# Optimization experiments

Hardware: AMD Instinct MI355X
Metric: run time of the kernel (lower is better)

The kernel has to match this reference:

```python
import jax, jax.numpy as jnp
import numpy as np

H = 2048
N = 2_097_152
BINS = 256


def _tensor2image(x):
    # de-normalize from [-1,1]-style to [0,1] (SCGAN's tensor2image)
    return x * 0.5 + 0.5


def _cdf(vals):
    # torch.histc(vals, bins=256, min=0, max=256): unit-width bins; values here lie in [0,256)
    b = jnp.clip(jnp.floor(vals), 0, BINS - 1).astype(jnp.int32)
    hist = jnp.zeros((BINS,), jnp.float32).at[b].add(1.0)
    c = jnp.cumsum(hist)
    return c / c[BINS - 1]


def _trans_table(ref_cdf, adj_cdf):
    # table[i] = first j in 1..255 with adj[j-1] <= ref[i] <= adj[j]; else i. table[0]=0, table[255]=255.
    r = ref_cdf[:, None]                # [256,1]
    lo = adj_cdf[None, :-1]             # adj[j-1], j=1..255
    hi = adj_cdf[None, 1:]              # adj[j]
    cond = (lo <= r) & (r <= hi)        # [256,255]
    found = jnp.any(cond, axis=1)
    j_first = 1 + jnp.argmax(cond, axis=1)
    table = jnp.where(found, j_first, jnp.arange(BINS))
    table = table.at[0].set(0).at[BINS - 1].set(BINS - 1)
    return table


def _histogram_matching(dst_img, ref_img, i0, i1, i2, i3):
    dst_align = dst_img[:, i0, i1]      # [3,N]
    ref_align = ref_img[:, i2, i3]      # [3,N]
    cdf_dst = jax.vmap(_cdf)(dst_align)           # [3,256]
    cdf_ref = jax.vmap(_cdf)(ref_align)           # [3,256]
    tables = jax.vmap(_trans_table)(cdf_dst, cdf_ref)  # [3,256] int
    ix = jnp.clip(jnp.floor(dst_align), 0, BINS - 1).astype(jnp.int32)
    matched = jnp.take_along_axis(tables, ix, axis=1).astype(dst_img.dtype)  # [3,N]
    return dst_img.at[:, i0, i1].set(matched)


def setup_inputs() -> dict:
    key = jax.random.key(0)
    ks = jax.random.split(key, 9)
    return {
        "input_data": jax.random.uniform(ks[0], (1, 3, H, H), jnp.float32),
        "target_data": jax.random.uniform(ks[1], (1, 3, H, H), jnp.float32),
        "mask_src": jax.random.randint(ks[2], (1, 1, H, H), 0, 2).astype(jnp.float32),
        "mask_tar": jax.random.randint(ks[3], (1, 1, H, H), 0, 2).astype(jnp.float32),
        "idx0": jax.random.randint(ks[4], (N,), 0, H),
        "idx1": jax.random.randint(ks[5], (N,), 0, H),
        "idx2": jax.random.randint(ks[6], (N,), 0, H),
        "idx3": jax.random.randint(ks[7], (N,), 0, H),
        "ref": jax.random.uniform(ks[8], (1, 3, H, H), jnp.float32),
    }


def reference(input_data, target_data, mask_src, mask_tar, idx0, idx1, idx2, idx3, ref):
    img = _tensor2image(input_data)[0] * 255.0   # [3,H,H]
    tgt = _tensor2image(target_data)[0] * 255.0  # [3,H,H]
    rf = _tensor2image(ref)[0] * 255.0           # [3,H,H]
    m_src = jnp.broadcast_to(mask_src[0, 0], img.shape)
    m_tar = jnp.broadcast_to(mask_tar[0, 0], tgt.shape)
    input_masked = img * m_src
    target_masked = tgt * m_tar
    ref_masked = rf * m_src
    match = jax.lax.stop_gradient(
        _histogram_matching(ref_masked, target_masked, idx0, idx1, idx2, idx3)
    ) * m_src
    return jnp.mean(jnp.abs(input_masked - match))
```

## Files before the change

### kernel.cpp

```cpp
#include <hip/hip_runtime.h>

#define H 2048
#define HH (H * H)
#define NIDX 2097152
#define BINS 256
#define CH 3

#define NBUCK 64
#define NLIST 128
#define CAPG  139264
#define WS_HIST_DST 0
#define WS_HIST_REF 3072
#define WS_TABLE    6144
#define WS_ACC      9216
#define WS_CURS     9728
#define WS_CTRL_BYTES 16384
#define WS_SEL      16384
#define WS_BPS      (16384 + (size_t)HH)
#define WS_BPR      (WS_BPS + (size_t)HH * 4)
#define WS_LIST     (WS_BPR + (size_t)HH * 4)
#define WS_MAIN_BYTES (WS_LIST + (size_t)NLIST * CAPG * 2)

#define FB_CNT_DST  16384
#define FB_BINPACK  (16384 + (size_t)HH * 2)
#define FB_ZERO_BYTES (16384 + (size_t)HH * 2)

__device__ __forceinline__ int bin_of(float v) {
    int b = (int)floorf(v);
    return min(max(b, 0), BINS - 1);
}


__global__ __launch_bounds__(256) void prep_main(
    const float* __restrict__ mask_src, const float* __restrict__ mask_tar,
    const float* __restrict__ refimg, const float* __restrict__ tgtimg,
    unsigned int* __restrict__ bps, unsigned int* __restrict__ bpr,
    unsigned int* __restrict__ sel4)
{
    const int nq = HH / 4;
    const int stride = gridDim.x * 256;
    for (int q = blockIdx.x * 256 + threadIdx.x; q < nq; q += stride) {
        float4 ms4 = ((const float4*)mask_src)[q];
        float4 mt4 = ((const float4*)mask_tar)[q];
        const float ms[4] = { ms4.x, ms4.y, ms4.z, ms4.w };
        const float mt[4] = { mt4.x, mt4.y, mt4.z, mt4.w };
        unsigned int wsrc[4] = { 0u, 0u, 0u, 0u };
        unsigned int wref[4] = { 0u, 0u, 0u, 0u };
        #pragma unroll
        for (int c = 0; c < CH; ++c) {
            float4 r4 = ((const float4*)(refimg + (size_t)c * HH))[q];
            float4 t4 = ((const float4*)(tgtimg + (size_t)c * HH))[q];
            const float rr[4] = { r4.x, r4.y, r4.z, r4.w };
            const float tt[4] = { t4.x, t4.y, t4.z, t4.w };
            #pragma unroll
            for (int e = 0; e < 4; ++e) {
                float vs = (rr[e] * 0.5f + 0.5f) * 255.0f * ms[e];
                float vt = (tt[e] * 0.5f + 0.5f) * 255.0f * mt[e];
                wsrc[e] |= ((unsigned int)bin_of(vs)) << (8 * c);
                wref[e] |= ((unsigned int)bin_of(vt)) << (8 * c);
            }
        }
        uint4 o1 = { wsrc[0], wsrc[1], wsrc[2], wsrc[3] };
        uint4 o2 = { wref[0], wref[1], wref[2], wref[3] };
        ((uint4*)bps)[q] = o1;
        ((uint4*)bpr)[q] = o2;
        sel4[q] = 0u;
    }
}

#define P1_BLOCKS 512
#define P1_SPB (NIDX / P1_BLOCKS)
#define P1_CAP 128

__global__ __launch_bounds__(256) void partition_kernel(
    const int* __restrict__ idx0, const int* __restrict__ idx1,
    const int* __restrict__ idx2, const int* __restrict__ idx3,
    unsigned short* __restrict__ list_g, unsigned int* __restrict__ curs)
{
    __shared__ unsigned short stage[NLIST * P1_CAP];
    __shared__ unsigned int lcnt[NLIST];
    __shared__ unsigned int lbase[NLIST];
    for (int i = threadIdx.x; i < NLIST; i += 256) lcnt[i] = 0u;
    __syncthreads();

    const int base_k = blockIdx.x * P1_SPB;
    for (int r = 0; r < P1_SPB / 256; ++r) {
        int k = base_k + r * 256 + threadIdx.x;
        int pd = idx0[k] * H + idx1[k];
        int pr = idx2[k] * H + idx3[k];
        {
            int l = pd >> 16;
            unsigned int pos = atomicAdd(&lcnt[l], 1u);
            if (pos < P1_CAP) stage[l * P1_CAP + pos] = (unsigned short)(pd & 0xFFFF);
            else {
                unsigned int g = atomicAdd(&curs[l], 1u);
                if (g < CAPG) list_g[(size_t)l * CAPG + g] = (unsigned short)(pd & 0xFFFF);
            }
        }
        {
            int l = 64 + (pr >> 16);
            unsigned int pos = atomicAdd(&lcnt[l], 1u);
            if (pos < P1_CAP) stage[l * P1_CAP + pos] = (unsigned short)(pr & 0xFFFF);
            else {
                unsigned int g = atomicAdd(&curs[l], 1u);
                if (g < CAPG) list_g[(size_t)l * CAPG + g] = (unsigned short)(pr & 0xFFFF);
            }
        }
    }
    __syncthreads();
    if (threadIdx.x < NLIST) {
        unsigned int n = min(lcnt[threadIdx.x], (unsigned int)P1_CAP);
        lbase[threadIdx.x] = atomicAdd(&curs[threadIdx.x], n);
    }
    __syncthreads();
    for (int b = 0; b < NLIST; ++b) {
        int n = (int)min(lcnt[b], (unsigned int)P1_CAP);
        unsigned int gb = lbase[b];
        for (int e = threadIdx.x; e < n; e += 256) {
            unsigned int gi = gb + e;
            if (gi < CAPG) list_g[(size_t)b * CAPG + gi] = stage[b * P1_CAP + e];
        }
    }
}

__global__ __launch_bounds__(256) void gather_hist_kernel(
    const unsigned short* __restrict__ list_g, const unsigned int* __restrict__ curs,
    const unsigned int* __restrict__ bps, const unsigned int* __restrict__ bpr,
    unsigned char* __restrict__ selected,
    unsigned int* __restrict__ hist_dst, unsigned int* __restrict__ hist_ref)
{
    __shared__ unsigned int hd[CH * BINS];
    __shared__ unsigned int hr[CH * BINS];
    for (int i = threadIdx.x; i < CH * BINS; i += 256) { hd[i] = 0u; hr[i] = 0u; }
    __syncthreads();

    const int xcd = blockIdx.x & 7;
    const int j = blockIdx.x >> 3;
    unsigned int zc_d = 0, zc_r = 0;

    for (int phase = 0; phase < 8; ++phase) {
        const int bucket = xcd * 8 + phase;
        const unsigned int pbase = ((unsigned int)bucket) << 16;
        {
            const int l = bucket;
            unsigned int n = min(curs[l], (unsigned int)CAPG);
            unsigned int chunk = (n + 255u) >> 8;
            unsigned int s = j * chunk;
            unsigned int e = min(s + chunk, n);
            for (unsigned int i = s + threadIdx.x; i < e; i += 256) {
                unsigned int p = pbase | (unsigned int)list_g[(size_t)l * CAPG + i];
                unsigned int w = bps[p];
                selected[p] = 1;
                if (w == 0u) ++zc_d;
                else {
                    atomicAdd(&hd[0 * BINS + (w & 0xFFu)], 1u);
                    atomicAdd(&hd[1 * BINS + ((w >> 8) & 0xFFu)], 1u);
                    atomicAdd(&hd[2 * BINS + ((w >> 16) & 0xFFu)], 1u);
                }
            }
        }
        {
            const int l = 64 + bucket;
            unsigned int n = min(curs[l], (unsigned int)CAPG);
            unsigned int chunk = (n + 255u) >> 8;
            unsigned int s = j * chunk;
            unsigned int e = min(s + chunk, n);
            for (unsigned int i = s + threadIdx.x; i < e; i += 256) {
                unsigned int p = pbase | (unsigned int)list_g[(size_t)l * CAPG + i];
                unsigned int w = bpr[p];
                if (w == 0u) ++zc_r;
                else {
                    atomicAdd(&hr[0 * BINS + (w & 0xFFu)], 1u);
                    atomicAdd(&hr[1 * BINS + ((w >> 8) & 0xFFu)], 1u);
                    atomicAdd(&hr[2 * BINS + ((w >> 16) & 0xFFu)], 1u);
                }
            }
        }
    }

    int zd = (int)zc_d, zr = (int)zc_r;
    #pragma unroll
    for (int off = 32; off; off >>= 1) { zd += __shfl_down(zd, off); zr += __shfl_down(zr, off); }
    if ((threadIdx.x & 63) == 0) {
        if (zd) {
            atomicAdd(&hd[0 * BINS], (unsigned int)zd);
            atomicAdd(&hd[1 * BINS], (unsigned int)zd);
            atomicAdd(&hd[2 * BINS], (unsigned int)zd);
        }
        if (zr) {
            atomicAdd(&hr[0 * BINS], (unsigned int)zr);
            atomicAdd(&hr[1 * BINS], (unsigned int)zr);
            atomicAdd(&hr[2 * BINS], (unsigned int)zr);
        }
    }

    __syncthreads();
    for (int i = threadIdx.x; i < CH * BINS; i += 256) {
        unsigned int v = hd[i];
        if (v) atomicAdd(&hist_dst[i], v);
        v = hr[i];
        if (v) atomicAdd(&hist_ref[i], v);
    }
}

__global__ __launch_bounds__(256) void table_kernel(
    const unsigned int* __restrict__ hist_dst,
    const unsigned int* __restrict__ hist_ref,
    int* __restrict__ table)
{
    __shared__ float cd[CH * BINS];
    __shared__ float cr[CH * BINS];
    __shared__ float wpart[4];
    const int i = threadIdx.x;
    const int lane = i & 63;
    const int wave = i >> 6;

    for (int a = 0; a < 6; ++a) {
        const unsigned int* h = (a < 3) ? (hist_dst + a * BINS) : (hist_ref + (a - 3) * BINS);
        float* out = (a < 3) ? (cd + a * BINS) : (cr + (a - 3) * BINS);
        float x = (float)h[i];
        #pragma unroll
        for (int off = 1; off < 64; off <<= 1) {
            float y = __shfl_up(x, off);
            if (lane >= off) x += y;
        }
        if (lane == 63) wpart[wave] = x;
        __syncthreads();
        float prefix = 0.0f;
        #pragma unroll
        for (int w = 0; w < 3; ++w) if (w < wave) prefix += wpart[w];
        x += prefix;
        float tot = wpart[0] + wpart[1] + wpart[2] + wpart[3];
        out[i] = x / tot;
        __syncthreads();
    }

    #pragma unroll
    for (int c = 0; c < CH; ++c) {
        int t;
        if (i == 0) t = 0;
        else if (i == BINS - 1) t = BINS - 1;
        else {
            float r = cd[c * BINS + i];
            int lo = 1, hi = BINS - 1;
            while (lo < hi) {
                int mid = (lo + hi) >> 1;
                if (cr[c * BINS + mid] < r) lo = mid + 1; else hi = mid;
            }
            t = (cr[c * BINS + lo - 1] <= r) ? lo : i;
        }
        table[c * BINS + i] = t;
    }
}

__global__ __launch_bounds__(256) void loss_sel_kernel(
    const float* __restrict__ input, const float* __restrict__ refimg,
    const float* __restrict__ mask_src, const unsigned char* __restrict__ selected,
    const int* __restrict__ table, double* __restrict__ acc)
{
    __shared__ int tab[CH * BINS];
    for (int i = threadIdx.x; i < CH * BINS; i += 256) tab[i] = table[i];
    __syncthreads();

    float lsum = 0.0f;
    const int nq = HH / 4;
    const int stride = gridDim.x * 256;
    for (int q = blockIdx.x * 256 + threadIdx.x; q < nq; q += stride) {
        float4 m4 = ((const float4*)mask_src)[q];
        uchar4 s4 = ((const uchar4*)selected)[q];
        const unsigned char ss[4] = { s4.x, s4.y, s4.z, s4.w };
        const float mm[4] = { m4.x, m4.y, m4.z, m4.w };
        #pragma unroll
        for (int c = 0; c < CH; ++c) {
            float4 a4 = ((const float4*)(input + (size_t)c * HH))[q];
            float4 r4 = ((const float4*)(refimg + (size_t)c * HH))[q];
            const float aa[4] = { a4.x, a4.y, a4.z, a4.w };
            const float rr[4] = { r4.x, r4.y, r4.z, r4.w };
            #pragma unroll
            for (int e = 0; e < 4; ++e) {
                float m = mm[e];
                float av = (aa[e] * 0.5f + 0.5f) * 255.0f * m;
                float rv = (rr[e] * 0.5f + 0.5f) * 255.0f * m;
                float tv = (float)tab[c * BINS + bin_of(rv)];
                float mv = m * (ss[e] ? tv : rv);
                lsum += fabsf(av - mv);
            }
        }
    }

    double d = (double)lsum;
    #pragma unroll
    for (int off = 32; off; off >>= 1) d += __shfl_down(d, off);
    __shared__ double wsum[4];
    int wid = threadIdx.x >> 6;
    int lane = threadIdx.x & 63;
    if (lane == 0) wsum[wid] = d;
    __syncthreads();
    if (threadIdx.x == 0) {
        double t = wsum[0] + wsum[1] + wsum[2] + wsum[3];
        atomicAdd(acc, t);
    }
}

__global__ void finalize_kernel(const double* __restrict__ acc, float* __restrict__ out)
{
    if (threadIdx.x == 0 && blockIdx.x == 0) {
        out[0] = (float)(acc[0] / (double)(CH * (double)HH));
    }
}


__device__ __forceinline__ void cnt_inc(unsigned int* cnt, int p) {
    atomicAdd(&cnt[p >> 1], (p & 1) ? 0x10000u : 1u);
}

__global__ __launch_bounds__(256) void fb_prep_kernel(
    const float* __restrict__ mask_tar, const float* __restrict__ tgtimg,
    unsigned int* __restrict__ binpack)
{
    const int nq = HH / 4;
    const int stride = gridDim.x * 256;
    for (int q = blockIdx.x * 256 + threadIdx.x; q < nq; q += stride) {
        float4 m4 = ((const float4*)mask_tar)[q];
        const float mm[4] = { m4.x, m4.y, m4.z, m4.w };
        unsigned int w[4] = { 0u, 0u, 0u, 0u };
        #pragma unroll
        for (int c = 0; c < CH; ++c) {
            float4 t4 = ((const float4*)(tgtimg + (size_t)c * HH))[q];
            const float tt[4] = { t4.x, t4.y, t4.z, t4.w };
            #pragma unroll
            for (int e = 0; e < 4; ++e) {
                float v = (tt[e] * 0.5f + 0.5f) * 255.0f * mm[e];
                w[e] |= ((unsigned int)bin_of(v)) << (8 * c);
            }
        }
        uint4 out = { w[0], w[1], w[2], w[3] };
        ((uint4*)binpack)[q] = out;
    }
}

__global__ __launch_bounds__(256) void fb_scatter_kernel(
    const int4* __restrict__ idx0, const int4* __restrict__ idx1,
    const int4* __restrict__ idx2, const int4* __restrict__ idx3,
    const unsigned int* __restrict__ binpack,
    unsigned int* __restrict__ cnt_dst, unsigned int* __restrict__ hist_ref)
{
    __shared__ unsigned int hr[CH * BINS];
    for (int i = threadIdx.x; i < CH * BINS; i += 256) hr[i] = 0u;
    __syncthreads();

    unsigned int zc = 0;
    const int n4 = NIDX / 4;
    const int stride = gridDim.x * 256;
    for (int k = blockIdx.x * 256 + threadIdx.x; k < n4; k += stride) {
        int4 a = idx0[k], b = idx1[k], c = idx2[k], d = idx3[k];
        int p0 = c.x * H + d.x, p1 = c.y * H + d.y;
        int p2 = c.z * H + d.z, p3 = c.w * H + d.w;
        unsigned int w0 = binpack[p0], w1 = binpack[p1];
        unsigned int w2 = binpack[p2], w3 = binpack[p3];

        cnt_inc(cnt_dst, a.x * H + b.x);
        cnt_inc(cnt_dst, a.y * H + b.y);
        cnt_inc(cnt_dst, a.z * H + b.z);
        cnt_inc(cnt_dst, a.w * H + b.w);

        const unsigned int ws2[4] = { w0, w1, w2, w3 };
        #pragma unroll
        for (int e = 0; e < 4; ++e) {
            unsigned int w = ws2[e];
            if (w == 0u) ++zc;
            else {
                atomicAdd(&hr[0 * BINS + (w & 0xFFu)], 1u);
                atomicAdd(&hr[1 * BINS + ((w >> 8) & 0xFFu)], 1u);
                atomicAdd(&hr[2 * BINS + ((w >> 16) & 0xFFu)], 1u);
            }
        }
    }

    int z = (int)zc;
    #pragma unroll
    for (int off = 32; off; off >>= 1) z += __shfl_down(z, off);
    if ((threadIdx.x & 63) == 0 && z) {
        atomicAdd(&hr[0 * BINS], (unsigned int)z);
        atomicAdd(&hr[1 * BINS], (unsigned int)z);
        atomicAdd(&hr[2 * BINS], (unsigned int)z);
    }

    __syncthreads();
    for (int i = threadIdx.x; i < CH * BINS; i += 256) {
        unsigned int v = hr[i];
        if (v) atomicAdd(&hist_ref[i], v);
    }
}

__global__ __launch_bounds__(256) void fb_sweep_kernel(
    const float* __restrict__ mask_src, const float* __restrict__ refimg,
    const unsigned int* __restrict__ cnt_dst,
    unsigned int* __restrict__ hist_dst)
{
    __shared__ unsigned int hd[CH * BINS];
    for (int i = threadIdx.x; i < CH * BINS; i += 256) hd[i] = 0u;
    __syncthreads();

    unsigned int zc = 0;
    const int nq = HH / 4;
    const int stride = gridDim.x * 256;
    for (int q = blockIdx.x * 256 + threadIdx.x; q < nq; q += stride) {
        uint2 wd = ((const uint2*)cnt_dst)[q];
        unsigned int cdc[4] = { wd.x & 0xFFFFu, wd.x >> 16, wd.y & 0xFFFFu, wd.y >> 16 };
        float4 ms4 = ((const float4*)mask_src)[q];
        const float ms[4] = { ms4.x, ms4.y, ms4.z, ms4.w };

        float rv[CH][4];
        #pragma unroll
        for (int c = 0; c < CH; ++c) {
            float4 r4 = ((const float4*)(refimg + (size_t)c * HH))[q];
            rv[c][0] = r4.x; rv[c][1] = r4.y; rv[c][2] = r4.z; rv[c][3] = r4.w;
        }
        #pragma unroll
        for (int e = 0; e < 4; ++e) {
            if (cdc[e]) {
                if (ms[e] == 0.0f) zc += cdc[e];
                else {
                    #pragma unroll
                    for (int c = 0; c < CH; ++c) {
                        float v = (rv[c][e] * 0.5f + 0.5f) * 255.0f;
                        atomicAdd(&hd[c * BINS + bin_of(v)], cdc[e]);
                    }
                }
            }
        }
    }

    int z = (int)zc;
    #pragma unroll
    for (int off = 32; off; off >>= 1) z += __shfl_down(z, off);
    if ((threadIdx.x & 63) == 0 && z) {
        atomicAdd(&hd[0 * BINS], (unsigned int)z);
        atomicAdd(&hd[1 * BINS], (unsigned int)z);
        atomicAdd(&hd[2 * BINS], (unsigned int)z);
    }

    __syncthreads();
    for (int i = threadIdx.x; i < CH * BINS; i += 256) {
        unsigned int v = hd[i];
        if (v) atomicAdd(&hist_dst[i], v);
    }
}

__global__ __launch_bounds__(256) void fb_loss_kernel(
    const float* __restrict__ input, const float* __restrict__ refimg,
    const float* __restrict__ mask_src, const unsigned int* __restrict__ cnt_dst,
    const int* __restrict__ table, double* __restrict__ acc)
{
    __shared__ int tab[CH * BINS];
    for (int i = threadIdx.x; i < CH * BINS; i += 256) tab[i] = table[i];
    __syncthreads();

    float lsum = 0.0f;
    const int nq = HH / 4;
    const int stride = gridDim.x * 256;
    for (int q = blockIdx.x * 256 + threadIdx.x; q < nq; q += stride) {
        float4 m4 = ((const float4*)mask_src)[q];
        uint2 w = ((const uint2*)cnt_dst)[q];
        const unsigned int sel[4] = { w.x & 0xFFFFu, w.x >> 16, w.y & 0xFFFFu, w.y >> 16 };
        const float mm[4] = { m4.x, m4.y, m4.z, m4.w };
        #pragma unroll
        for (int c = 0; c < CH; ++c) {
            float4 a4 = ((const float4*)(input + (size_t)c * HH))[q];
            float4 r4 = ((const float4*)(refimg + (size_t)c * HH))[q];
            const float aa[4] = { a4.x, a4.y, a4.z, a4.w };
            const float rr[4] = { r4.x, r4.y, r4.z, r4.w };
            #pragma unroll
            for (int e = 0; e < 4; ++e) {
                float m = mm[e];
                float av = (aa[e] * 0.5f + 0.5f) * 255.0f * m;
                float rv = (rr[e] * 0.5f + 0.5f) * 255.0f * m;
                float tv = (float)tab[c * BINS + bin_of(rv)];
                float mv = m * (sel[e] ? tv : rv);
                lsum += fabsf(av - mv);
            }
        }
    }

    double d = (double)lsum;
    #pragma unroll
    for (int off = 32; off; off >>= 1) d += __shfl_down(d, off);
    __shared__ double wsum[4];
    int wid = threadIdx.x >> 6;
    int lane = threadIdx.x & 63;
    if (lane == 0) wsum[wid] = d;
    __syncthreads();
    if (threadIdx.x == 0) {
        double t = wsum[0] + wsum[1] + wsum[2] + wsum[3];
        atomicAdd(acc, t);
    }
}


extern "C" void kernel_launch(void* const* d_in, const int* in_sizes, int n_in,
                              void* d_out, int out_size, void* d_ws, size_t ws_size,
                              hipStream_t stream)
{
    const float* input    = (const float*)d_in[0];
    const float* target   = (const float*)d_in[1];
    const float* mask_src = (const float*)d_in[2];
    const float* mask_tar = (const float*)d_in[3];
    const int*   idx0     = (const int*)d_in[4];
    const int*   idx1     = (const int*)d_in[5];
    const int*   idx2     = (const int*)d_in[6];
    const int*   idx3     = (const int*)d_in[7];
    const float* refimg   = (const float*)d_in[8];

    char* ws = (char*)d_ws;
    unsigned int* hist_dst = (unsigned int*)(ws + WS_HIST_DST);
    unsigned int* hist_ref = (unsigned int*)(ws + WS_HIST_REF);
    int*          table    = (int*)(ws + WS_TABLE);
    double*       acc      = (double*)(ws + WS_ACC);

    if (ws_size >= WS_MAIN_BYTES) {
        unsigned int*   curs     = (unsigned int*)(ws + WS_CURS);
        unsigned char*  selected = (unsigned char*)(ws + WS_SEL);
        unsigned int*   bps      = (unsigned int*)(ws + WS_BPS);
        unsigned int*   bpr      = (unsigned int*)(ws + WS_BPR);
        unsigned short* list_g   = (unsigned short*)(ws + WS_LIST);

        hipMemsetAsync(d_ws, 0, WS_CTRL_BYTES, stream);
        prep_main<<<2048, 256, 0, stream>>>(mask_src, mask_tar, refimg, target,
                                            bps, bpr, (unsigned int*)selected);
        partition_kernel<<<P1_BLOCKS, 256, 0, stream>>>(idx0, idx1, idx2, idx3,
                                                        list_g, curs);
        gather_hist_kernel<<<2048, 256, 0, stream>>>(list_g, curs, bps, bpr,
                                                     selected, hist_dst, hist_ref);
        table_kernel<<<1, 256, 0, stream>>>(hist_dst, hist_ref, table);
        loss_sel_kernel<<<2048, 256, 0, stream>>>(input, refimg, mask_src,
                                                  selected, table, acc);
        finalize_kernel<<<1, 64, 0, stream>>>(acc, (float*)d_out);
    } else {
        unsigned int* cnt_dst = (unsigned int*)(ws + FB_CNT_DST);
        unsigned int* binpack = (unsigned int*)(ws + FB_BINPACK);

        hipMemsetAsync(d_ws, 0, FB_ZERO_BYTES, stream);
        fb_prep_kernel<<<2048, 256, 0, stream>>>(mask_tar, target, binpack);
        fb_scatter_kernel<<<2048, 256, 0, stream>>>((const int4*)idx0, (const int4*)idx1,
                                                    (const int4*)idx2, (const int4*)idx3,
                                                    binpack, cnt_dst, hist_ref);
        fb_sweep_kernel<<<1024, 256, 0, stream>>>(mask_src, refimg, cnt_dst, hist_dst);
        table_kernel<<<1, 256, 0, stream>>>(hist_dst, hist_ref, table);
        fb_loss_kernel<<<2048, 256, 0, stream>>>(input, refimg, mask_src, cnt_dst,
                                                 table, acc);
        finalize_kernel<<<1, 64, 0, stream>>>(acc, (float*)d_out);
    }
}
```

Baseline: 351.1 us.

## Split gather-histogram work per block by side and bucket with vectorized list loads

New measurement: 328.5 us. -6.4%, faster.

```diff
diff --git a/kernel.cpp b/kernel.cpp
--- a/kernel.cpp
+++ b/kernel.cpp
@@ -129,77 +129,81 @@
     unsigned char* __restrict__ selected,
     unsigned int* __restrict__ hist_dst, unsigned int* __restrict__ hist_ref)
 {
-    __shared__ unsigned int hd[CH * BINS];
-    __shared__ unsigned int hr[CH * BINS];
-    for (int i = threadIdx.x; i < CH * BINS; i += 256) { hd[i] = 0u; hr[i] = 0u; }
-    __syncthreads();
-
-    const int xcd = blockIdx.x & 7;
-    const int j = blockIdx.x >> 3;
-    unsigned int zc_d = 0, zc_r = 0;
-
-    for (int phase = 0; phase < 8; ++phase) {
-        const int bucket = xcd * 8 + phase;
-        const unsigned int pbase = ((unsigned int)bucket) << 16;
-        {
-            const int l = bucket;
-            unsigned int n = min(curs[l], (unsigned int)CAPG);
-            unsigned int chunk = (n + 255u) >> 8;
-            unsigned int s = j * chunk;
-            unsigned int e = min(s + chunk, n);
-            for (unsigned int i = s + threadIdx.x; i < e; i += 256) {
-                unsigned int p = pbase | (unsigned int)list_g[(size_t)l * CAPG + i];
-                unsigned int w = bps[p];
-                selected[p] = 1;
-                if (w == 0u) ++zc_d;
+    __shared__ unsigned int hh[CH * BINS];
+    for (int i = threadIdx.x; i < CH * BINS; i += 256) hh[i] = 0u;
+    __syncthreads();
+
+    const int xcd  = blockIdx.x & 7;
+    const int j    = blockIdx.x >> 3;
+    const int bsl  = j & 15;
+    const int sub  = j >> 4;
+    const int side = bsl >> 3;
+    const int bucket = xcd * 8 + (bsl & 7);
+    const int l = side * 64 + bucket;
+    const unsigned int pbase = ((unsigned int)bucket) << 16;
+    const unsigned int* __restrict__ src = side ? bpr : bps;
+
+    const unsigned int n = min(curs[l], (unsigned int)CAPG);
+    const unsigned int chunk = (((n + 15u) >> 4) + 7u) & ~7u;
+    const unsigned int s = (unsigned int)sub * chunk;
+    const unsigned int e = min(s + chunk, n);
+    const unsigned short* lbase = list_g + (size_t)l * CAPG;
+
+    unsigned int zc = 0;
+    for (unsigned int ib = s + (unsigned int)threadIdx.x * 8u; ib < e; ib += 2048u) {
+        unsigned int w[8];
+        unsigned int pcnt;
+        if (ib + 8u <= e) {
+            uint4 raw = *(const uint4*)(lbase + ib);
+            const unsigned int ent[8] = {
+                raw.x & 0xFFFFu, raw.x >> 16, raw.y & 0xFFFFu, raw.y >> 16,
+                raw.z & 0xFFFFu, raw.z >> 16, raw.w & 0xFFFFu, raw.w >> 16 };
+            #pragma unroll
+            for (int k = 0; k < 8; ++k) {
+                unsigned int p = pbase | ent[k];
+                w[k] = src[p];
+                if (side == 0) selected[p] = 1;
+            }
+            pcnt = 8u;
+        } else {
+            pcnt = e - ib;
+            #pragma unroll
+            for (int k = 0; k < 8; ++k) {
+                if ((unsigned int)k < pcnt) {
+                    unsigned int p = pbase | (unsigned int)lbase[ib + k];
+                    w[k] = src[p];
+                    if (side == 0) selected[p] = 1;
+                } else w[k] = 0xFFFFFFFFu;
+            }
+        }
+        #pragma unroll
+        for (int k = 0; k < 8; ++k) {
+            if ((unsigned int)k < pcnt) {
+                unsigned int ww = w[k];
+                if (ww == 0u) ++zc;
                 else {
-                    atomicAdd(&hd[0 * BINS + (w & 0xFFu)], 1u);
-                    atomicAdd(&hd[1 * BINS + ((w >> 8) & 0xFFu)], 1u);
-                    atomicAdd(&hd[2 * BINS + ((w >> 16) & 0xFFu)], 1u);
+                    atomicAdd(&hh[0 * BINS + (ww & 0xFFu)], 1u);
+                    atomicAdd(&hh[1 * BINS + ((ww >> 8) & 0xFFu)], 1u);
+                    atomicAdd(&hh[2 * BINS + ((ww >> 16) & 0xFFu)], 1u);
                 }
             }
         }
-        {
-            const int l = 64 + bucket;
-            unsigned int n = min(curs[l], (unsigned int)CAPG);
-            unsigned int chunk = (n + 255u) >> 8;
-            unsigned int s = j * chunk;
-            unsigned int e = min(s + chunk, n);
-            for (unsigned int i = s + threadIdx.x; i < e; i += 256) {
-                unsigned int p = pbase | (unsigned int)list_g[(size_t)l * CAPG + i];
-                unsigned int w = bpr[p];
-                if (w == 0u) ++zc_r;
-                else {
-                    atomicAdd(&hr[0 * BINS + (w & 0xFFu)], 1u);
-                    atomicAdd(&hr[1 * BINS + ((w >> 8) & 0xFFu)], 1u);
-                    atomicAdd(&hr[2 * BINS + ((w >> 16) & 0xFFu)], 1u);
-                }
-            }
-        }
-    }
-
-    int zd = (int)zc_d, zr = (int)zc_r;
+    }
+
+    int z = (int)zc;
     #pragma unroll
-    for (int off = 32; off; off >>= 1) { zd += __shfl_down(zd, off); zr += __shfl_down(zr, off); }
-    if ((threadIdx.x & 63) == 0) {
-        if (zd) {
-            atomicAdd(&hd[0 * BINS], (unsigned int)zd);
-            atomicAdd(&hd[1 * BINS], (unsigned int)zd);
-            atomicAdd(&hd[2 * BINS], (unsigned int)zd);
-        }
-        if (zr) {
-            atomicAdd(&hr[0 * BINS], (unsigned int)zr);
-            atomicAdd(&hr[1 * BINS], (unsigned int)zr);
-            atomicAdd(&hr[2 * BINS], (unsigned int)zr);
-        }
-    }
-
-    __syncthreads();
+    for (int off = 32; off; off >>= 1) z += __shfl_down(z, off);
+    if ((threadIdx.x & 63) == 0 && z) {
+        atomicAdd(&hh[0 * BINS], (unsigned int)z);
+        atomicAdd(&hh[1 * BINS], (unsigned int)z);
+        atomicAdd(&hh[2 * BINS], (unsigned int)z);
+    }
+
+    __syncthreads();
+    unsigned int* dsthist = side ? hist_ref : hist_dst;
     for (int i = threadIdx.x; i < CH * BINS; i += 256) {
-        unsigned int v = hd[i];
-        if (v) atomicAdd(&hist_dst[i], v);
-        v = hr[i];
-        if (v) atomicAdd(&hist_ref[i], v);
+        unsigned int v = hh[i];
+        if (v) atomicAdd(&dsthist[i], v);
     }
 }
 
```
